# Kernel tuning notes

Measured on AMD Instinct MI355X. Metric: run time of the kernel, lower is better.

The kernel has to match this reference:

```python
import jax, jax.numpy as jnp
import numpy as np

E, H, I, K = 8, 1024, 768, 2
T = 2048  # flattened batch*seq tokens

def setup_inputs() -> dict:
    key = jax.random.key(0)
    k1, k2, k3, k4, k5 = jax.random.split(key, 5)
    hidden_states = jax.random.normal(k1, (T, H), dtype=jnp.float32)
    gate_up_proj = jax.random.normal(k2, (E, 2 * I, H), dtype=jnp.float32) * 0.02
    down_proj = jax.random.normal(k3, (E, H, I), dtype=jnp.float32) * 0.02
    top_k_index = jax.random.randint(k4, (T, K), 0, E)
    top_k_weights = jax.nn.softmax(jax.random.normal(k5, (T, K), dtype=jnp.float32), axis=-1)
    return {
        "hidden_states": hidden_states,
        "gate_up_proj": gate_up_proj,
        "down_proj": down_proj,
        "top_k_index": top_k_index,
        "top_k_weights": top_k_weights,
    }


def reference(hidden_states, gate_up_proj, down_proj, top_k_index, top_k_weights):
    # hidden_states: [T, H]; gate_up_proj: [E, 2I, H]; down_proj: [E, H, I]
    # top_k_index: [T, K] int; top_k_weights: [T, K] float
    num_experts = gate_up_proj.shape[0]
    # Combine weights per (token, expert): zero for unrouted experts, so the
    # dense-over-experts compute below yields exactly the routed MoE output.
    onehot = jax.nn.one_hot(top_k_index, num_experts, dtype=hidden_states.dtype)  # [T, K, E]
    combine = jnp.einsum("tke,tk->te", onehot, top_k_weights)  # [T, E]
    # Grouped GEMM 1: fused gate+up projection for all experts.
    gu = jnp.einsum("th,eoh->teo", hidden_states, gate_up_proj)  # [T, E, 2I]
    inter = gu.shape[-1] // 2
    gate, up = gu[..., :inter], gu[..., inter:]
    h = jax.nn.silu(gate) * up  # [T, E, I]
    # Grouped GEMM 2: down projection.
    expert_out = jnp.einsum("tei,ehi->teh", h, down_proj)  # [T, E, H]
    return jnp.einsum("teh,te->th", expert_out, combine)  # [T, H]
```

## Files before the change

kernel.cpp:

```cpp
#include <hip/hip_runtime.h>
#include <hip/hip_bf16.h>

#define T_TOK   2048
#define NEXP    8
#define HDIM    1024
#define IDIM    768
#define TOPK    2
#define NASSIGN (T_TOK*TOPK)
#define MT      128
#define MAX_TILES 40
#define SLOT_PAD 5120

typedef unsigned short u16;
typedef unsigned int   u32;

typedef __bf16 bf16x8 __attribute__((ext_vector_type(8)));
typedef float  f32x4  __attribute__((ext_vector_type(4)));

struct Meta {
  int n_tiles;
  int _pad[15];
  int tile_e[80];
  int tile_m[80];
  int tile_n[80];
};

__device__ __forceinline__ u16 f2bf(float f) {
  u32 x = __float_as_uint(f);
  return (u16)((x + 0x7fffu + ((x >> 16) & 1u)) >> 16);
}

__device__ __forceinline__ int4 pack8(const float* __restrict__ p) {
  float4 a = *(const float4*)p;
  float4 b = *(const float4*)(p + 4);
  union { u16 u[8]; int4 v; } r;
  r.u[0] = f2bf(a.x); r.u[1] = f2bf(a.y); r.u[2] = f2bf(a.z); r.u[3] = f2bf(a.w);
  r.u[4] = f2bf(b.x); r.u[5] = f2bf(b.y); r.u[6] = f2bf(b.z); r.u[7] = f2bf(b.w);
  return r.v;
}

__device__ __forceinline__ bf16x8 asbf(int4 v) {
  return __builtin_bit_cast(bf16x8, v);
}

__device__ __forceinline__ void gll(const void* g, void* l) {
  __builtin_amdgcn_global_load_lds(
      (const __attribute__((address_space(1))) u32*)g,
      (__attribute__((address_space(3))) u32*)l, 16, 0, 0);
}

__global__ __launch_bounds__(256) void prep_k(
    const float* __restrict__ hs, const float* __restrict__ gup,
    const float* __restrict__ down, const int* __restrict__ topk,
    const float* __restrict__ tw,
    u16* __restrict__ hs16, u16* __restrict__ gup16, u16* __restrict__ down16,
    Meta* __restrict__ meta, int* __restrict__ slot_token, float* __restrict__ slot_w,
    float* __restrict__ out) {
  int tid = threadIdx.x;

  if (blockIdx.x == 0) {
    __shared__ int s_cnt[NEXP], s_off[NEXP], s_cur[NEXP];
    if (tid < NEXP) { s_cnt[tid] = 0; s_cur[tid] = 0; }
    __syncthreads();
    for (int i = tid; i < NASSIGN; i += 256)
      atomicAdd(&s_cnt[topk[i]], 1);
    __syncthreads();
    if (tid == 0) {
      int acc = 0, nt = 0;
      for (int e = 0; e < NEXP; ++e) {
        s_off[e] = acc;
        int c = s_cnt[e];
        for (int mb = 0; mb < c; mb += MT) {
          meta->tile_e[nt] = e;
          meta->tile_m[nt] = acc + mb;
          meta->tile_n[nt] = (c - mb) < MT ? (c - mb) : MT;
          ++nt;
        }
        acc += c;
      }
      meta->n_tiles = nt;
    }
    __syncthreads();
    for (int i = tid; i < NASSIGN; i += 256) {
      int e = topk[i];
      int p = s_off[e] + atomicAdd(&s_cur[e], 1);
      slot_token[p] = i / TOPK;
      slot_w[p]     = tw[i];
    }
    for (int i = NASSIGN + tid; i < SLOT_PAD; i += 256) {
      slot_token[i] = 0;
      slot_w[i]     = 0.0f;
    }
    return;
  }

  const size_t NTH = 512 * 256;
  size_t t = ((size_t)blockIdx.x - 1) * 256 + tid;

  #pragma unroll
  for (int k = 0; k < 12; ++k) {
    size_t i = t + (size_t)k * NTH;
    *(int4*)(gup16 + i * 8) = pack8(gup + i * 8);
  }
  #pragma unroll
  for (int k = 0; k < 6; ++k) {
    size_t i = t + (size_t)k * NTH;
    *(int4*)(down16 + i * 8) = pack8(down + i * 8);
  }
  #pragma unroll
  for (int k = 0; k < 2; ++k) {
    size_t i = t + (size_t)k * NTH;
    *(int4*)(hs16 + i * 8) = pack8(hs + i * 8);
  }
  int4 z = {0, 0, 0, 0};
  #pragma unroll
  for (int k = 0; k < 4; ++k) {
    size_t i = t + (size_t)k * NTH;
    *(int4*)(out + i * 4) = z;
  }
}

__global__ __launch_bounds__(512, 2) void gemm1_k(
    const u16* __restrict__ hs16, const u16* __restrict__ gup16,
    const Meta* __restrict__ meta, const int* __restrict__ slot_token,
    const float* __restrict__ slot_w, u16* __restrict__ hbuf) {
  int bid = blockIdx.x;
  int wg = (bid & 7) * 30 + (bid >> 3);
  int tile = wg / 6, y = wg % 6;
  if (tile >= meta->n_tiles) return;
  int e = meta->tile_e[tile], mbase = meta->tile_m[tile], nrows = meta->tile_n[tile];
  int n0 = y * 128;

  __shared__ int4 lds[3][3][1024];
  int tid = threadIdx.x, lane = tid & 63, w = tid >> 6;
  int wm = w >> 2, wn = w & 3;
  f32x4 accg[4][2] = {}, accu[4][2] = {};

  const u16* gb = gup16 + (size_t)e * (2 * IDIM) * HDIM + (size_t)n0 * HDIM;
  const u16* ub = gb + (size_t)IDIM * HDIM;

  int c0 = tid, c1 = tid + 512;
  int r0 = c0 >> 3, s0 = (c0 & 7) ^ (r0 & 7);
  int r1 = c1 >> 3, s1 = (c1 & 7) ^ (r1 & 7);
  const u16* a0 = hs16 + (size_t)slot_token[mbase + r0] * HDIM + s0 * 8;
  const u16* a1 = hs16 + (size_t)slot_token[mbase + r1] * HDIM + s1 * 8;
  const u16* g0 = gb + (size_t)r0 * HDIM + s0 * 8;
  const u16* g1 = gb + (size_t)r1 * HDIM + s1 * 8;
  const u16* u0 = ub + (size_t)r0 * HDIM + s0 * 8;
  const u16* u1 = ub + (size_t)r1 * HDIM + s1 * 8;

  auto STAGE = [&](int b, int k0) {
    gll(a0 + k0, &lds[b][0][w * 64]);
    gll(a1 + k0, &lds[b][0][512 + w * 64]);
    gll(g0 + k0, &lds[b][1][w * 64]);
    gll(g1 + k0, &lds[b][1][512 + w * 64]);
    gll(u0 + k0, &lds[b][2][w * 64]);
    gll(u1 + k0, &lds[b][2][512 + w * 64]);
  };

  STAGE(0, 0);
  STAGE(1, 64);
  #pragma unroll
  for (int kt = 0; kt < 16; ++kt) {
    __builtin_amdgcn_s_barrier();
    if (kt + 2 < 16) STAGE((kt + 2) % 3, (kt + 2) * 64);
    if (kt < 14)       asm volatile("s_waitcnt vmcnt(12)" ::: "memory");
    else if (kt == 14) asm volatile("s_waitcnt vmcnt(6)" ::: "memory");
    else               asm volatile("s_waitcnt vmcnt(0)" ::: "memory");
    __builtin_amdgcn_sched_barrier(0);
    const int cur = kt % 3;
    #pragma unroll
    for (int ks = 0; ks < 2; ++ks) {
      bf16x8 af[4], bgf[2], buf_[2];
      int slot = ks * 4 + (lane >> 4);
      #pragma unroll
      for (int i = 0; i < 4; ++i) {
        int row = wm * 64 + i * 16 + (lane & 15);
        af[i] = asbf(lds[cur][0][(row << 3) | (slot ^ (row & 7))]);
      }
      #pragma unroll
      for (int j = 0; j < 2; ++j) {
        int row = wn * 32 + j * 16 + (lane & 15);
        int idx = (row << 3) | (slot ^ (row & 7));
        bgf[j]  = asbf(lds[cur][1][idx]);
        buf_[j] = asbf(lds[cur][2][idx]);
      }
      #pragma unroll
      for (int i = 0; i < 4; ++i)
        #pragma unroll
        for (int j = 0; j < 2; ++j) {
          accg[i][j] = __builtin_amdgcn_mfma_f32_16x16x32_bf16(af[i], bgf[j],  accg[i][j], 0, 0, 0);
          accu[i][j] = __builtin_amdgcn_mfma_f32_16x16x32_bf16(af[i], buf_[j], accu[i][j], 0, 0, 0);
        }
    }
  }

  int fq = lane >> 4, fr = lane & 15;
  #pragma unroll
  for (int i = 0; i < 4; ++i)
    #pragma unroll
    for (int r = 0; r < 4; ++r) {
      int row = wm * 64 + i * 16 + fq * 4 + r;
      if (row < nrows) {
        float wgt = slot_w[mbase + row];
        #pragma unroll
        for (int j = 0; j < 2; ++j) {
          float g = accg[i][j][r], u = accu[i][j][r];
          float s = g / (1.0f + __expf(-g));
          hbuf[(size_t)(mbase + row) * IDIM + n0 + wn * 32 + j * 16 + fr] = f2bf(s * u * wgt);
        }
      }
    }
}

__global__ __launch_bounds__(512, 4) void gemm2_k(
    const u16* __restrict__ hbuf, const u16* __restrict__ down16,
    const Meta* __restrict__ meta, const int* __restrict__ slot_token,
    float* __restrict__ out) {
  int bid = blockIdx.x;
  int wg = (bid & 7) * 40 + (bid >> 3);
  int tile = wg / 8, y = wg % 8;
  if (tile >= meta->n_tiles) return;
  int e = meta->tile_e[tile], mbase = meta->tile_m[tile], nrows = meta->tile_n[tile];
  int n0 = y * 128;

  __shared__ int4 lds[2][2][1024];
  int tid = threadIdx.x, lane = tid & 63, w = tid >> 6;
  int wm = w >> 2, wn = w & 3;
  f32x4 acc[4][2] = {};
  const u16* db = down16 + (size_t)e * HDIM * IDIM + (size_t)n0 * IDIM;

  int c0 = tid, c1 = tid + 512;
  int r0 = c0 >> 3, s0 = (c0 & 7) ^ (r0 & 7);
  int r1 = c1 >> 3, s1 = (c1 & 7) ^ (r1 & 7);
  const u16* a0 = hbuf + (size_t)(mbase + r0) * IDIM + s0 * 8;
  const u16* a1 = hbuf + (size_t)(mbase + r1) * IDIM + s1 * 8;
  const u16* b0 = db + (size_t)r0 * IDIM + s0 * 8;
  const u16* b1 = db + (size_t)r1 * IDIM + s1 * 8;

  auto STAGE = [&](int b, int k0) {
    gll(a0 + k0, &lds[b][0][w * 64]);
    gll(a1 + k0, &lds[b][0][512 + w * 64]);
    gll(b0 + k0, &lds[b][1][w * 64]);
    gll(b1 + k0, &lds[b][1][512 + w * 64]);
  };

  STAGE(0, 0);
  #pragma unroll
  for (int kt = 0; kt < 12; ++kt) {
    __builtin_amdgcn_s_barrier();
    if (kt + 1 < 12) STAGE((kt + 1) & 1, (kt + 1) * 64);
    if (kt < 11) asm volatile("s_waitcnt vmcnt(4)" ::: "memory");
    else         asm volatile("s_waitcnt vmcnt(0)" ::: "memory");
    __builtin_amdgcn_sched_barrier(0);
    const int cur = kt & 1;
    #pragma unroll
    for (int ks = 0; ks < 2; ++ks) {
      bf16x8 af[4], bf[2];
      int slot = ks * 4 + (lane >> 4);
      #pragma unroll
      for (int i = 0; i < 4; ++i) {
        int row = wm * 64 + i * 16 + (lane & 15);
        af[i] = asbf(lds[cur][0][(row << 3) | (slot ^ (row & 7))]);
      }
      #pragma unroll
      for (int j = 0; j < 2; ++j) {
        int row = wn * 32 + j * 16 + (lane & 15);
        bf[j] = asbf(lds[cur][1][(row << 3) | (slot ^ (row & 7))]);
      }
      #pragma unroll
      for (int i = 0; i < 4; ++i)
        #pragma unroll
        for (int j = 0; j < 2; ++j)
          acc[i][j] = __builtin_amdgcn_mfma_f32_16x16x32_bf16(af[i], bf[j], acc[i][j], 0, 0, 0);
    }
  }

  int fq = lane >> 4, fr = lane & 15;
  #pragma unroll
  for (int i = 0; i < 4; ++i)
    #pragma unroll
    for (int r = 0; r < 4; ++r) {
      int row = wm * 64 + i * 16 + fq * 4 + r;
      if (row < nrows) {
        int tok = slot_token[mbase + row];
        #pragma unroll
        for (int j = 0; j < 2; ++j)
          atomicAdd(out + (size_t)tok * HDIM + n0 + wn * 32 + j * 16 + fr, acc[i][j][r]);
      }
    }
}

extern "C" void kernel_launch(void* const* d_in, const int* in_sizes, int n_in,
                              void* d_out, int out_size, void* d_ws, size_t ws_size,
                              hipStream_t stream) {
  const float* hs   = (const float*)d_in[0];
  const float* gup  = (const float*)d_in[1];
  const float* down = (const float*)d_in[2];
  const int*   topk = (const int*)d_in[3];
  const float* tw   = (const float*)d_in[4];
  float* out = (float*)d_out;

  const size_t o_hs16   = 65536;
  const size_t o_hbuf   = o_hs16 + (size_t)T_TOK * HDIM * 2;
  const size_t o_gup16  = o_hbuf + (size_t)SLOT_PAD * IDIM * 2;
  const size_t o_down16 = o_gup16 + (size_t)NEXP * 2 * IDIM * HDIM * 2;
  const size_t needed   = o_down16 + (size_t)NEXP * HDIM * IDIM * 2;

  char* ws = (char*)d_ws;
  Meta*  meta       = (Meta*)ws;
  int*   slot_token = (int*)(ws + 4096);
  float* slot_w     = (float*)(ws + 24576);
  u16*   hs16       = (u16*)(ws + o_hs16);
  u16*   hbuf       = (u16*)(ws + o_hbuf);
  u16*   gup16      = (u16*)(ws + o_gup16);
  u16*   down16     = (u16*)(ws + o_down16);

  if (ws_size < needed) return;

  prep_k<<<513, 256, 0, stream>>>(hs, gup, down, topk, tw,
                                  hs16, gup16, down16, meta, slot_token, slot_w, out);
  gemm1_k<<<MAX_TILES * 6, 512, 0, stream>>>(hs16, gup16, meta, slot_token, slot_w, hbuf);
  gemm2_k<<<MAX_TILES * 8, 512, 0, stream>>>(hbuf, down16, meta, slot_token, out);
}
```

Before: 177.7 us.

## Fuse fp32-to-bf16 conversion of inputs and weights into GEMM tile loads

Drops the separate pre-pass that converted hidden states, gate_up and down weights to bf16 in workspace. The GEMM kernels now load fp32 straight into registers, convert, and write swizzled bf16 tiles to LDS, with register prefetch overlapping the MFMA work. This removes a full read plus write of all weights and activations. The cost is twice the global bytes per tile load, with fp32 weights re-read by every M-tile. The pipeline also drops from three LDS stages with async global-to-LDS loads to two stages, and occupancy hints are lowered.

Result: slower. 198.3 us (+11.6%).

```diff
diff --git a/kernel.cpp b/kernel.cpp
--- a/kernel.cpp
+++ b/kernel.cpp
@@ -30,9 +30,7 @@
   return (u16)((x + 0x7fffu + ((x >> 16) & 1u)) >> 16);
 }
 
-__device__ __forceinline__ int4 pack8(const float* __restrict__ p) {
-  float4 a = *(const float4*)p;
-  float4 b = *(const float4*)(p + 4);
+__device__ __forceinline__ int4 cvt8r(float4 a, float4 b) {
   union { u16 u[8]; int4 v; } r;
   r.u[0] = f2bf(a.x); r.u[1] = f2bf(a.y); r.u[2] = f2bf(a.z); r.u[3] = f2bf(a.w);
   r.u[4] = f2bf(b.x); r.u[5] = f2bf(b.y); r.u[6] = f2bf(b.z); r.u[7] = f2bf(b.w);
@@ -50,14 +48,10 @@
 }
 
 __global__ __launch_bounds__(256) void prep_k(
-    const float* __restrict__ hs, const float* __restrict__ gup,
-    const float* __restrict__ down, const int* __restrict__ topk,
-    const float* __restrict__ tw,
-    u16* __restrict__ hs16, u16* __restrict__ gup16, u16* __restrict__ down16,
+    const int* __restrict__ topk, const float* __restrict__ tw,
     Meta* __restrict__ meta, int* __restrict__ slot_token, float* __restrict__ slot_w,
     float* __restrict__ out) {
   int tid = threadIdx.x;
-
   if (blockIdx.x == 0) {
     __shared__ int s_cnt[NEXP], s_off[NEXP], s_cur[NEXP];
     if (tid < NEXP) { s_cnt[tid] = 0; s_cur[tid] = 0; }
@@ -93,35 +87,15 @@
     }
     return;
   }
-
-  const size_t NTH = 512 * 256;
   size_t t = ((size_t)blockIdx.x - 1) * 256 + tid;
-
-  #pragma unroll
-  for (int k = 0; k < 12; ++k) {
-    size_t i = t + (size_t)k * NTH;
-    *(int4*)(gup16 + i * 8) = pack8(gup + i * 8);
-  }
-  #pragma unroll
-  for (int k = 0; k < 6; ++k) {
-    size_t i = t + (size_t)k * NTH;
-    *(int4*)(down16 + i * 8) = pack8(down + i * 8);
-  }
-  #pragma unroll
-  for (int k = 0; k < 2; ++k) {
-    size_t i = t + (size_t)k * NTH;
-    *(int4*)(hs16 + i * 8) = pack8(hs + i * 8);
-  }
   int4 z = {0, 0, 0, 0};
   #pragma unroll
-  for (int k = 0; k < 4; ++k) {
-    size_t i = t + (size_t)k * NTH;
-    *(int4*)(out + i * 4) = z;
-  }
-}
-
-__global__ __launch_bounds__(512, 2) void gemm1_k(
-    const u16* __restrict__ hs16, const u16* __restrict__ gup16,
+  for (int k = 0; k < 8; ++k)
+    *(int4*)(out + (t + (size_t)k * 65536) * 4) = z;
+}
+
+__global__ __launch_bounds__(512, 1) void gemm1_k(
+    const float* __restrict__ hs, const float* __restrict__ gup,
     const Meta* __restrict__ meta, const int* __restrict__ slot_token,
     const float* __restrict__ slot_w, u16* __restrict__ hbuf) {
   int bid = blockIdx.x;
@@ -131,44 +105,46 @@
   int e = meta->tile_e[tile], mbase = meta->tile_m[tile], nrows = meta->tile_n[tile];
   int n0 = y * 128;
 
-  __shared__ int4 lds[3][3][1024];
+  __shared__ int4 lds[2][3][1024];
   int tid = threadIdx.x, lane = tid & 63, w = tid >> 6;
   int wm = w >> 2, wn = w & 3;
   f32x4 accg[4][2] = {}, accu[4][2] = {};
 
-  const u16* gb = gup16 + (size_t)e * (2 * IDIM) * HDIM + (size_t)n0 * HDIM;
-  const u16* ub = gb + (size_t)IDIM * HDIM;
-
-  int c0 = tid, c1 = tid + 512;
-  int r0 = c0 >> 3, s0 = (c0 & 7) ^ (r0 & 7);
-  int r1 = c1 >> 3, s1 = (c1 & 7) ^ (r1 & 7);
-  const u16* a0 = hs16 + (size_t)slot_token[mbase + r0] * HDIM + s0 * 8;
-  const u16* a1 = hs16 + (size_t)slot_token[mbase + r1] * HDIM + s1 * 8;
-  const u16* g0 = gb + (size_t)r0 * HDIM + s0 * 8;
-  const u16* g1 = gb + (size_t)r1 * HDIM + s1 * 8;
-  const u16* u0 = ub + (size_t)r0 * HDIM + s0 * 8;
-  const u16* u1 = ub + (size_t)r1 * HDIM + s1 * 8;
-
-  auto STAGE = [&](int b, int k0) {
-    gll(a0 + k0, &lds[b][0][w * 64]);
-    gll(a1 + k0, &lds[b][0][512 + w * 64]);
-    gll(g0 + k0, &lds[b][1][w * 64]);
-    gll(g1 + k0, &lds[b][1][512 + w * 64]);
-    gll(u0 + k0, &lds[b][2][w * 64]);
-    gll(u1 + k0, &lds[b][2][512 + w * 64]);
+  int r0 = tid >> 3, s = tid & 7;
+  int tok0 = slot_token[mbase + r0];
+  int tok1 = slot_token[mbase + r0 + 64];
+  const float* A0 = hs + (size_t)tok0 * HDIM + s * 8;
+  const float* A1 = hs + (size_t)tok1 * HDIM + s * 8;
+  const float* G0 = gup + (size_t)e * (2 * IDIM) * HDIM + (size_t)(n0 + r0) * HDIM + s * 8;
+  const float* G1 = G0 + (size_t)64 * HDIM;
+  const float* U0 = G0 + (size_t)IDIM * HDIM;
+  const float* U1 = G1 + (size_t)IDIM * HDIM;
+  const int i0 = (r0 << 3) | (s ^ (r0 & 7));
+  const int i1 = ((r0 + 64) << 3) | (s ^ (r0 & 7));
+
+  float4 v[12];
+  auto LOADS = [&](int k0) {
+    v[0]  = *(const float4*)(A0 + k0); v[1]  = *(const float4*)(A0 + k0 + 4);
+    v[2]  = *(const float4*)(A1 + k0); v[3]  = *(const float4*)(A1 + k0 + 4);
+    v[4]  = *(const float4*)(G0 + k0); v[5]  = *(const float4*)(G0 + k0 + 4);
+    v[6]  = *(const float4*)(G1 + k0); v[7]  = *(const float4*)(G1 + k0 + 4);
+    v[8]  = *(const float4*)(U0 + k0); v[9]  = *(const float4*)(U0 + k0 + 4);
+    v[10] = *(const float4*)(U1 + k0); v[11] = *(const float4*)(U1 + k0 + 4);
   };
-
-  STAGE(0, 0);
-  STAGE(1, 64);
-  #pragma unroll
+  auto CVTWRITE = [&](int b) {
+    lds[b][0][i0] = cvt8r(v[0], v[1]);   lds[b][0][i1] = cvt8r(v[2], v[3]);
+    lds[b][1][i0] = cvt8r(v[4], v[5]);   lds[b][1][i1] = cvt8r(v[6], v[7]);
+    lds[b][2][i0] = cvt8r(v[8], v[9]);   lds[b][2][i1] = cvt8r(v[10], v[11]);
+  };
+
+  LOADS(0);
+  CVTWRITE(0);
+  #pragma unroll 1
   for (int kt = 0; kt < 16; ++kt) {
-    __builtin_amdgcn_s_barrier();
-    if (kt + 2 < 16) STAGE((kt + 2) % 3, (kt + 2) * 64);
-    if (kt < 14)       asm volatile("s_waitcnt vmcnt(12)" ::: "memory");
-    else if (kt == 14) asm volatile("s_waitcnt vmcnt(6)" ::: "memory");
-    else               asm volatile("s_waitcnt vmcnt(0)" ::: "memory");
+    __syncthreads();
+    if (kt < 15) LOADS((kt + 1) * 64);
     __builtin_amdgcn_sched_barrier(0);
-    const int cur = kt % 3;
+    const int cur = kt & 1;
     #pragma unroll
     for (int ks = 0; ks < 2; ++ks) {
       bf16x8 af[4], bgf[2], buf_[2];
@@ -193,6 +169,7 @@
           accu[i][j] = __builtin_amdgcn_mfma_f32_16x16x32_bf16(af[i], buf_[j], accu[i][j], 0, 0, 0);
         }
     }
+    if (kt < 15) CVTWRITE((kt + 1) & 1);
   }
 
   int fq = lane >> 4, fr = lane & 15;
@@ -206,15 +183,15 @@
         #pragma unroll
         for (int j = 0; j < 2; ++j) {
           float g = accg[i][j][r], u = accu[i][j][r];
-          float s = g / (1.0f + __expf(-g));
-          hbuf[(size_t)(mbase + row) * IDIM + n0 + wn * 32 + j * 16 + fr] = f2bf(s * u * wgt);
+          float sg = g / (1.0f + __expf(-g));
+          hbuf[(size_t)(mbase + row) * IDIM + n0 + wn * 32 + j * 16 + fr] = f2bf(sg * u * wgt);
         }
       }
     }
 }
 
-__global__ __launch_bounds__(512, 4) void gemm2_k(
-    const u16* __restrict__ hbuf, const u16* __restrict__ down16,
+__global__ __launch_bounds__(512, 2) void gemm2_k(
+    const u16* __restrict__ hbuf, const float* __restrict__ down,
     const Meta* __restrict__ meta, const int* __restrict__ slot_token,
     float* __restrict__ out) {
   int bid = blockIdx.x;
@@ -228,30 +205,37 @@
   int tid = threadIdx.x, lane = tid & 63, w = tid >> 6;
   int wm = w >> 2, wn = w & 3;
   f32x4 acc[4][2] = {};
-  const u16* db = down16 + (size_t)e * HDIM * IDIM + (size_t)n0 * IDIM;
 
   int c0 = tid, c1 = tid + 512;
-  int r0 = c0 >> 3, s0 = (c0 & 7) ^ (r0 & 7);
-  int r1 = c1 >> 3, s1 = (c1 & 7) ^ (r1 & 7);
-  const u16* a0 = hbuf + (size_t)(mbase + r0) * IDIM + s0 * 8;
-  const u16* a1 = hbuf + (size_t)(mbase + r1) * IDIM + s1 * 8;
-  const u16* b0 = db + (size_t)r0 * IDIM + s0 * 8;
-  const u16* b1 = db + (size_t)r1 * IDIM + s1 * 8;
-
-  auto STAGE = [&](int b, int k0) {
+  int rA0 = c0 >> 3, sA0 = (c0 & 7) ^ (rA0 & 7);
+  int rA1 = c1 >> 3, sA1 = (c1 & 7) ^ (rA1 & 7);
+  const u16* a0 = hbuf + (size_t)(mbase + rA0) * IDIM + sA0 * 8;
+  const u16* a1 = hbuf + (size_t)(mbase + rA1) * IDIM + sA1 * 8;
+
+  int r0 = tid >> 3, s = tid & 7;
+  const float* B0 = down + (size_t)e * HDIM * IDIM + (size_t)(n0 + r0) * IDIM + s * 8;
+  const float* B1 = B0 + (size_t)64 * IDIM;
+  const int i0 = (r0 << 3) | (s ^ (r0 & 7));
+  const int i1 = ((r0 + 64) << 3) | (s ^ (r0 & 7));
+
+  float4 vb[4];
+  auto LOADS = [&](int b, int k0) {
     gll(a0 + k0, &lds[b][0][w * 64]);
     gll(a1 + k0, &lds[b][0][512 + w * 64]);
-    gll(b0 + k0, &lds[b][1][w * 64]);
-    gll(b1 + k0, &lds[b][1][512 + w * 64]);
+    vb[0] = *(const float4*)(B0 + k0); vb[1] = *(const float4*)(B0 + k0 + 4);
+    vb[2] = *(const float4*)(B1 + k0); vb[3] = *(const float4*)(B1 + k0 + 4);
   };
-
-  STAGE(0, 0);
-  #pragma unroll
+  auto CVTWRITE = [&](int b) {
+    lds[b][1][i0] = cvt8r(vb[0], vb[1]);
+    lds[b][1][i1] = cvt8r(vb[2], vb[3]);
+  };
+
+  LOADS(0, 0);
+  CVTWRITE(0);
+  #pragma unroll 1
   for (int kt = 0; kt < 12; ++kt) {
-    __builtin_amdgcn_s_barrier();
-    if (kt + 1 < 12) STAGE((kt + 1) & 1, (kt + 1) * 64);
-    if (kt < 11) asm volatile("s_waitcnt vmcnt(4)" ::: "memory");
-    else         asm volatile("s_waitcnt vmcnt(0)" ::: "memory");
+    __syncthreads();
+    if (kt < 11) LOADS((kt + 1) & 1, (kt + 1) * 64);
     __builtin_amdgcn_sched_barrier(0);
     const int cur = kt & 1;
     #pragma unroll
@@ -274,6 +258,7 @@
         for (int j = 0; j < 2; ++j)
           acc[i][j] = __builtin_amdgcn_mfma_f32_16x16x32_bf16(af[i], bf[j], acc[i][j], 0, 0, 0);
     }
+    if (kt < 11) CVTWRITE((kt + 1) & 1);
   }
 
   int fq = lane >> 4, fr = lane & 15;
@@ -301,25 +286,15 @@
   const float* tw   = (const float*)d_in[4];
   float* out = (float*)d_out;
 
-  const size_t o_hs16   = 65536;
-  const size_t o_hbuf   = o_hs16 + (size_t)T_TOK * HDIM * 2;
-  const size_t o_gup16  = o_hbuf + (size_t)SLOT_PAD * IDIM * 2;
-  const size_t o_down16 = o_gup16 + (size_t)NEXP * 2 * IDIM * HDIM * 2;
-  const size_t needed   = o_down16 + (size_t)NEXP * HDIM * IDIM * 2;
-
   char* ws = (char*)d_ws;
   Meta*  meta       = (Meta*)ws;
   int*   slot_token = (int*)(ws + 4096);
   float* slot_w     = (float*)(ws + 24576);
-  u16*   hs16       = (u16*)(ws + o_hs16);
-  u16*   hbuf       = (u16*)(ws + o_hbuf);
-  u16*   gup16      = (u16*)(ws + o_gup16);
-  u16*   down16     = (u16*)(ws + o_down16);
-
+  u16*   hbuf       = (u16*)(ws + 65536);
+  const size_t needed = 65536 + (size_t)SLOT_PAD * IDIM * 2;
   if (ws_size < needed) return;
 
-  prep_k<<<513, 256, 0, stream>>>(hs, gup, down, topk, tw,
-                                  hs16, gup16, down16, meta, slot_token, slot_w, out);
-  gemm1_k<<<MAX_TILES * 6, 512, 0, stream>>>(hs16, gup16, meta, slot_token, slot_w, hbuf);
-  gemm2_k<<<MAX_TILES * 8, 512, 0, stream>>>(hbuf, down16, meta, slot_token, out);
-}
+  prep_k<<<257, 256, 0, stream>>>(topk, tw, meta, slot_token, slot_w, out);
+  gemm1_k<<<MAX_TILES * 6, 512, 0, stream>>>(hs, gup, meta, slot_token, slot_w, hbuf);
+  gemm2_k<<<MAX_TILES * 8, 512, 0, stream>>>(hbuf, down, meta, slot_token, out);
+}
```
